# Optimization experiments

Measured on AMD Instinct MI355X. Metric: run time of the kernel, lower is better.

The kernel has to match this reference:

```python
import jax, jax.numpy as jnp
import numpy as np

B, T, C, H = 4, 2048, 1024, 16


def setup_inputs() -> dict:
    key = jax.random.key(0)
    k0, k1, k2 = jax.random.split(key, 3)
    s = C ** -0.5
    return {
        "x": jax.random.normal(k0, (B, T, C), jnp.float32),
        "Wqkv": jax.random.normal(k1, (C, 3 * C), jnp.float32) * s,
        "bqkv": jnp.zeros((3 * C,), jnp.float32),
        "Wo": jax.random.normal(k2, (C, C), jnp.float32) * s,
        "bo": jnp.zeros((C,), jnp.float32),
        "decoder": 1,
    }


def reference(x, Wqkv, bqkv, Wo, bo, decoder):
    Bx, Tx, Cx = x.shape
    d = Cx // H  # head dim
    qkv = x @ Wqkv + bqkv  # [B,T,3C]
    q, k, v = jnp.split(qkv, 3, axis=-1)
    q = q.reshape(Bx, Tx, H, d).transpose(0, 2, 1, 3)  # [B,H,T,d]
    k = k.reshape(Bx, Tx, H, d).transpose(0, 2, 1, 3)
    v = v.reshape(Bx, Tx, H, d).transpose(0, 2, 1, 3)
    # Source: qk / embd_dim**(-0.5)  ==  qk * sqrt(embd_dim)  (faithful quirk)
    scale = jnp.asarray(Cx ** 0.5, x.dtype)
    qk = jnp.einsum("bhqd,bhkd->bhqk", q, k) * scale  # [B,H,T,T]
    if decoder:  # decoder is a Python int constant
        tril = jnp.tril(jnp.ones((Tx, Tx), bool))
        qk = jnp.where(tril, qk, -jnp.inf)
    attn = jax.nn.softmax(qk, axis=-1)
    out = jnp.einsum("bhqk,bhkd->bhqd", attn, v)  # [B,H,T,d]
    out = out.transpose(0, 2, 1, 3).reshape(Bx, Tx, Cx)
    return out @ Wo + bo
```

## Files before the change

### kernel.cpp

```cpp
#include <hip/hip_runtime.h>
#include <cstdint>
#include <cstddef>

#define T_SEQ 2048
#define CEMB  1024
#define NHEAD 16
#define DHEAD 64

#define QSCALE 46.1662413084468f

typedef __attribute__((ext_vector_type(8))) short bf16x8;
typedef __attribute__((ext_vector_type(4))) float f32x4;

static __device__ __forceinline__ unsigned short f2bf(float x) {
    unsigned u = __builtin_bit_cast(unsigned, x);
    unsigned r = (u + 0x7FFFu + ((u >> 16) & 1u)) >> 16;
    return (unsigned short)r;
}
static __device__ __forceinline__ float bf2f(unsigned short b) {
    unsigned u = ((unsigned)b) << 16;
    return __builtin_bit_cast(float, u);
}

static __device__ __forceinline__ void gload16(const short* gsrc, short* ldsbase) {
    __builtin_amdgcn_global_load_lds(
        (const __attribute__((address_space(1))) void*)gsrc,
        (__attribute__((address_space(3))) void*)ldsbase, 16, 0, 0);
}

template<int SPLIT, bool A_F32, int OUT_MODE>
__global__ __launch_bounds__(256) void gemm_mfma_kernel(
    const float* __restrict__ Af, const short* __restrict__ Ah,
    const short* __restrict__ Bh, const short* __restrict__ Bl,
    const float* __restrict__ bias,
    void* __restrict__ Cout, void* __restrict__ Cout2, int K, int ldc)
{
    __shared__ __align__(16) short smem[(SPLIT == 3) ? 16384 : 8192];

    const int tid = threadIdx.x;
    const int w = tid >> 6, l = tid & 63;
    const int lr = l & 15, lg = l >> 4;
    const int wr = w >> 1, wc = w & 1;
    const int row0 = blockIdx.y * 128;
    const int col0 = blockIdx.x * 128;

    f32x4 acc[4][4];
    #pragma unroll
    for (int mt = 0; mt < 4; ++mt)
        #pragma unroll
        for (int nt = 0; nt < 4; ++nt)
            acc[mt][nt] = (f32x4){0.f, 0.f, 0.f, 0.f};

    const int sB0 = w * 128 + l, sB1 = sB0 + 64;
    const short* gB0 = Bh + (size_t)(col0 + (sB0 & 127)) * K + (sB0 >> 7) * 8;
    const short* gB1 = Bh + (size_t)(col0 + (sB1 & 127)) * K + (sB1 >> 7) * 8;
    short* dB0 = &smem[4096 + (w * 128) * 8];
    short* dB1 = &smem[4096 + (w * 128 + 64) * 8];
    const short* gBl0 = nullptr; const short* gBl1 = nullptr;
    if constexpr (SPLIT == 3) {
        gBl0 = Bl + (size_t)(col0 + (sB0 & 127)) * K + (sB0 >> 7) * 8;
        gBl1 = Bl + (size_t)(col0 + (sB1 & 127)) * K + (sB1 >> 7) * 8;
    }
    const short* gA0 = nullptr; const short* gA1 = nullptr;
    if constexpr (!A_F32) {
        gA0 = Ah + (size_t)(row0 + (sB0 & 127)) * K + (sB0 >> 7) * 8;
        gA1 = Ah + (size_t)(row0 + (sB1 & 127)) * K + (sB1 >> 7) * 8;
    }
    short* dA0 = &smem[(w * 128) * 8];
    short* dA1 = &smem[(w * 128 + 64) * 8];

    const int arow = tid >> 1, ahalf = tid & 1;
    const float* gAf = A_F32 ? (Af + (size_t)(row0 + arow) * K + ahalf * 16) : nullptr;

    for (int kt = 0; kt < K; kt += 32) {
        __syncthreads();
        if constexpr (!A_F32) {
            gload16(gA0 + kt, dA0);
            gload16(gA1 + kt, dA1);
        }
        gload16(gB0 + kt, dB0);
        gload16(gB1 + kt, dB1);
        if constexpr (SPLIT == 3) {
            gload16(gBl0 + kt, &smem[12288 + (w * 128) * 8]);
            gload16(gBl1 + kt, &smem[12288 + (w * 128 + 64) * 8]);
        }
        if constexpr (A_F32) {
            const float* src = gAf + kt;
            float4 f0 = *(const float4*)(src);
            float4 f1 = *(const float4*)(src + 4);
            float4 f2 = *(const float4*)(src + 8);
            float4 f3 = *(const float4*)(src + 12);
            float xs[16] = {f0.x, f0.y, f0.z, f0.w, f1.x, f1.y, f1.z, f1.w,
                            f2.x, f2.y, f2.z, f2.w, f3.x, f3.y, f3.z, f3.w};
            #pragma unroll
            for (int q = 0; q < 2; ++q) {
                bf16x8 h8, l8;
                #pragma unroll
                for (int e = 0; e < 8; ++e) {
                    float x = xs[q * 8 + e];
                    if constexpr (SPLIT == 3) {
                        unsigned u = __builtin_bit_cast(unsigned, x);
                        h8[e] = (short)(unsigned short)(u >> 16);
                        float hf = __builtin_bit_cast(float, u & 0xFFFF0000u);
                        l8[e] = (short)f2bf(x - hf);
                    } else {
                        h8[e] = (short)f2bf(x);
                    }
                }
                int slot = (ahalf * 2 + q) * 128 + arow;
                *(bf16x8*)&smem[slot * 8] = h8;
                if constexpr (SPLIT == 3) *(bf16x8*)&smem[8192 + slot * 8] = l8;
            }
        }
        __syncthreads();

        const int aoff = (lg * 128 + wr * 64 + lr) * 8;
        const int boff = 4096 + (lg * 128 + wc * 64 + lr) * 8;
        bf16x8 ahf[4], alf[4];
        #pragma unroll
        for (int mt = 0; mt < 4; ++mt) {
            ahf[mt] = *(const bf16x8*)&smem[aoff + mt * 128];
            if constexpr (SPLIT == 3)
                alf[mt] = *(const bf16x8*)&smem[8192 + aoff + mt * 128];
        }
        #pragma unroll
        for (int nt = 0; nt < 4; ++nt) {
            bf16x8 bhf = *(const bf16x8*)&smem[boff + nt * 128];
            if constexpr (SPLIT == 3) {
                bf16x8 blf = *(const bf16x8*)&smem[8192 + boff + nt * 128];
                #pragma unroll
                for (int mt = 0; mt < 4; ++mt) {
                    acc[mt][nt] = __builtin_amdgcn_mfma_f32_16x16x32_bf16(ahf[mt], bhf, acc[mt][nt], 0, 0, 0);
                    acc[mt][nt] = __builtin_amdgcn_mfma_f32_16x16x32_bf16(alf[mt], bhf, acc[mt][nt], 0, 0, 0);
                    acc[mt][nt] = __builtin_amdgcn_mfma_f32_16x16x32_bf16(ahf[mt], blf, acc[mt][nt], 0, 0, 0);
                }
            } else {
                #pragma unroll
                for (int mt = 0; mt < 4; ++mt)
                    acc[mt][nt] = __builtin_amdgcn_mfma_f32_16x16x32_bf16(ahf[mt], bhf, acc[mt][nt], 0, 0, 0);
            }
        }
    }

    #pragma unroll
    for (int mt = 0; mt < 4; ++mt) {
        #pragma unroll
        for (int r = 0; r < 4; ++r) {
            int m = row0 + wr * 64 + mt * 16 + lg * 4 + r;
            #pragma unroll
            for (int nt = 0; nt < 4; ++nt) {
                int n = col0 + wc * 64 + nt * 16 + lr;
                float v = acc[mt][nt][r] + bias[n];
                if constexpr (OUT_MODE == 0) {
                    ((float*)Cout)[(size_t)m * ldc + n] = v;
                } else if constexpr (OUT_MODE == 1) {
                    ((short*)Cout)[(size_t)m * ldc + n] = (short)f2bf(v);
                } else {
                    if (n < 1024) v *= QSCALE;
                    unsigned u = __builtin_bit_cast(unsigned, v);
                    ((short*)Cout)[(size_t)m * ldc + n] = (short)(unsigned short)(u >> 16);
                    float hf = __builtin_bit_cast(float, u & 0xFFFF0000u);
                    ((short*)Cout2)[(size_t)m * ldc + n] = (short)f2bf(v - hf);
                }
            }
        }
    }
}

__global__ __launch_bounds__(256) void transpose_split_kernel(
    const float* __restrict__ src, int nsrc,
    short* __restrict__ hi, short* __restrict__ lo)
{
    __shared__ float tile[64][68];
    const int tid = threadIdx.x;
    const int n0 = blockIdx.x * 64, k0 = blockIdx.y * 64;
    {
        int kr = tid >> 2, cg = tid & 3;
        const float* s = src + (size_t)(k0 + kr) * nsrc + n0 + cg * 16;
        #pragma unroll
        for (int q = 0; q < 4; ++q) {
            float4 f = *(const float4*)(s + q * 4);
            tile[kr][cg * 16 + q * 4 + 0] = f.x;
            tile[kr][cg * 16 + q * 4 + 1] = f.y;
            tile[kr][cg * 16 + q * 4 + 2] = f.z;
            tile[kr][cg * 16 + q * 4 + 3] = f.w;
        }
    }
    __syncthreads();
    {
        int nr = tid >> 2, kg = tid & 3;
        int n = n0 + nr;
        bf16x8 h0, h1, lo0, lo1;
        #pragma unroll
        for (int e = 0; e < 8; ++e) {
            float a = tile[kg * 16 + e][nr];
            float b = tile[kg * 16 + 8 + e][nr];
            unsigned short ha = f2bf(a), hb = f2bf(b);
            h0[e] = (short)ha; h1[e] = (short)hb;
            lo0[e] = (short)f2bf(a - bf2f(ha));
            lo1[e] = (short)f2bf(b - bf2f(hb));
        }
        short* dh = hi + (size_t)n * 1024 + k0 + kg * 16;
        *(bf16x8*)dh = h0;
        *(bf16x8*)(dh + 8) = h1;
        if (lo) {
            short* dl = lo + (size_t)n * 1024 + k0 + kg * 16;
            *(bf16x8*)dl = lo0;
            *(bf16x8*)(dl + 8) = lo1;
        }
    }
}

__global__ __launch_bounds__(256) void repack_vt_kernel(
    const short* __restrict__ v, short* __restrict__ vt)
{
    __shared__ short tile[64][80];
    const int tid = threadIdx.x;
    const int tt = blockIdx.x, h = blockIdx.y, b = blockIdx.z;
    const int t0 = tt * 64;
    {
        int tr = tid >> 2, cgrp = tid & 3;
        const short* src = v + (size_t)(b * T_SEQ + t0 + tr) * CEMB + h * DHEAD + cgrp * 16;
        *(bf16x8*)&tile[tr][cgrp * 16]     = *(const bf16x8*)src;
        *(bf16x8*)&tile[tr][cgrp * 16 + 8] = *(const bf16x8*)(src + 8);
    }
    __syncthreads();
    {
        int d = tid >> 2, tc = tid & 3;
        short s[16];
        #pragma unroll
        for (int e = 0; e < 16; ++e) s[e] = tile[tc * 16 + e][d];
        short* dst = vt + ((size_t)((b * NHEAD + h) * DHEAD + d)) * T_SEQ + t0 + tc * 16;
        bf16x8 v0, v1;
        #pragma unroll
        for (int e = 0; e < 8; ++e) { v0[e] = s[e]; v1[e] = s[8 + e]; }
        *(bf16x8*)dst       = v0;
        *(bf16x8*)(dst + 8) = v1;
    }
}

__global__ __launch_bounds__(256) void attn_mfma_kernel(
    const short* __restrict__ qkhi, const short* __restrict__ qklo,
    const short* __restrict__ vt, short* __restrict__ ctxb)
{
    __shared__ __align__(16) short smem[16384];

    const int tid = threadIdx.x;
    const int w = tid >> 6, l = tid & 63;
    const int lr = l & 15, lg = l >> 4;

    const int bid = blockIdx.x;
    const int p  = bid >> 6;
    const int bh = bid & 63;
    const int h = bh & 15, b = bh >> 4;
    const size_t bT = (size_t)b * T_SEQ;

    const int g0 = w * 128 + l, g1 = g0 + 64;
    const int rg0 = g0 >> 3, rg1 = g1 >> 3;
    const int sc0 = (g0 & 7) ^ (rg0 & 7), sc1 = (g1 & 7) ^ (rg1 & 7);
    short* const dst0 = &smem[(w * 128) * 8];
    short* const dst1 = &smem[(w * 128 + 64) * 8];

    const size_t koff0 = (bT + rg0) * 2048 + 1024 + h * DHEAD + sc0 * 8;
    const size_t koff1 = (bT + rg1) * 2048 + 1024 + h * DHEAD + sc1 * 8;
    const short* const pKh0 = qkhi + koff0;
    const short* const pKh1 = qkhi + koff1;
    const short* const pKl0 = qklo + koff0;
    const short* const pKl1 = qklo + koff1;
    const short* const pV0 = vt + ((size_t)((b * NHEAD + h) * DHEAD) + rg0) * T_SEQ + sc0 * 8;
    const short* const pV1 = vt + ((size_t)((b * NHEAD + h) * DHEAD) + rg1) * T_SEQ + sc1 * 8;

    for (int half = 0; half < 2; ++half) {
        const int xi = half ? (31 - p) : p;
        const int q0 = xi * 64;
        const int qw = q0 + w * 16;

        bf16x8 ahi[2], alo[2];
        #pragma unroll
        for (int kk = 0; kk < 2; ++kk) {
            size_t off = (bT + qw + lr) * 2048 + h * DHEAD + kk * 32 + lg * 8;
            ahi[kk] = *(const bf16x8*)(qkhi + off);
            alo[kk] = *(const bf16x8*)(qklo + off);
        }

        f32x4 O[4];
        #pragma unroll
        for (int dt = 0; dt < 4; ++dt)
            O[dt] = (f32x4){0.f, 0.f, 0.f, 0.f};
        float mrun[4], lrun[4];
        #pragma unroll
        for (int r = 0; r < 4; ++r) { mrun[r] = -3.0e38f; lrun[r] = 0.f; }

        const int nsteps = xi + 1;
        for (int t = 0; t < nsteps; ++t) {
            const int j0 = t * 64;
            __syncthreads();
            gload16(pKh0 + (size_t)j0 * 2048, dst0);
            gload16(pKh1 + (size_t)j0 * 2048, dst1);
            gload16(pKl0 + (size_t)j0 * 2048, dst0 + 4096);
            gload16(pKl1 + (size_t)j0 * 2048, dst1 + 4096);
            gload16(pV0 + j0, dst0 + 8192);
            gload16(pV1 + j0, dst1 + 8192);
            __syncthreads();

            f32x4 S[4];
            #pragma unroll
            for (int ct = 0; ct < 4; ++ct) {
                f32x4 s = (f32x4){0.f, 0.f, 0.f, 0.f};
                #pragma unroll
                for (int kk = 0; kk < 2; ++kk) {
                    int j  = ct * 16 + lr;
                    int ck = kk * 4 + lg;
                    int idx = j * 64 + ((ck ^ (j & 7)) << 3);
                    bf16x8 bh8 = *(bf16x8*)&smem[idx];
                    bf16x8 bl8 = *(bf16x8*)&smem[4096 + idx];
                    s = __builtin_amdgcn_mfma_f32_16x16x32_bf16(ahi[kk], bh8, s, 0, 0, 0);
                    s = __builtin_amdgcn_mfma_f32_16x16x32_bf16(alo[kk], bh8, s, 0, 0, 0);
                    s = __builtin_amdgcn_mfma_f32_16x16x32_bf16(ahi[kk], bl8, s, 0, 0, 0);
                }
                if (j0 + ct * 16 + 15 > qw) {
                    int jabs = j0 + ct * 16 + lr;
                    #pragma unroll
                    for (int r = 0; r < 4; ++r) {
                        int qabs = qw + lg * 4 + r;
                        s[r] = (jabs <= qabs) ? s[r] : -3.0e38f;
                    }
                }
                S[ct] = s;
            }

            float tm[4];
            #pragma unroll
            for (int r = 0; r < 4; ++r) {
                float v = fmaxf(fmaxf(S[0][r], S[1][r]), fmaxf(S[2][r], S[3][r]));
                v = fmaxf(v, __shfl_xor(v, 1));
                v = fmaxf(v, __shfl_xor(v, 2));
                v = fmaxf(v, __shfl_xor(v, 4));
                v = fmaxf(v, __shfl_xor(v, 8));
                tm[r] = v;
            }
            bool exceed = (tm[0] > mrun[0]) | (tm[1] > mrun[1]) |
                          (tm[2] > mrun[2]) | (tm[3] > mrun[3]);
            if (__any(exceed)) {
                #pragma unroll
                for (int r = 0; r < 4; ++r) {
                    float mnew  = fmaxf(mrun[r], tm[r]);
                    float alpha = __builtin_amdgcn_exp2f(mrun[r] - mnew);
                    mrun[r] = mnew;
                    lrun[r] *= alpha;
                    #pragma unroll
                    for (int dt = 0; dt < 4; ++dt)
                        O[dt][r] *= alpha;
                }
            }

            float lsum[4] = {0.f, 0.f, 0.f, 0.f};
            #pragma unroll
            for (int ct = 0; ct < 4; ++ct) {
                #pragma unroll
                for (int r = 0; r < 4; ++r) {
                    float pv = __builtin_amdgcn_exp2f(S[ct][r] - mrun[r]);
                    lsum[r] += pv;
                    int row = lg * 4 + r;
                    int col = ct * 16 + lr;
                    smem[12288 + w * 1024 + row * 64 + (col ^ ((row & 7) << 3))] = (short)f2bf(pv);
                }
            }
            #pragma unroll
            for (int r = 0; r < 4; ++r) {
                float s = lsum[r];
                s += __shfl_xor(s, 1);
                s += __shfl_xor(s, 2);
                s += __shfl_xor(s, 4);
                s += __shfl_xor(s, 8);
                lrun[r] += s;
            }

            __builtin_amdgcn_wave_barrier();

            bf16x8 pa[2];
            #pragma unroll
            for (int jk = 0; jk < 2; ++jk) {
                int ck = jk * 4 + lg;
                pa[jk] = *(bf16x8*)&smem[12288 + w * 1024 + lr * 64 + ((ck ^ (lr & 7)) << 3)];
            }
            #pragma unroll
            for (int dt = 0; dt < 4; ++dt) {
                #pragma unroll
                for (int jk = 0; jk < 2; ++jk) {
                    int d  = dt * 16 + lr;
                    int ck = jk * 4 + lg;
                    bf16x8 vb = *(bf16x8*)&smem[8192 + d * 64 + ((ck ^ (d & 7)) << 3)];
                    O[dt] = __builtin_amdgcn_mfma_f32_16x16x32_bf16(pa[jk], vb, O[dt], 0, 0, 0);
                }
            }
        }

        #pragma unroll
        for (int r = 0; r < 4; ++r) {
            float inv = 1.0f / lrun[r];
            int row = qw + lg * 4 + r;
            #pragma unroll
            for (int dt = 0; dt < 4; ++dt) {
                int col = h * DHEAD + dt * 16 + lr;
                ctxb[(size_t)(b * T_SEQ + row) * CEMB + col] = (short)f2bf(O[dt][r] * inv);
            }
        }
    }
}

extern "C" void kernel_launch(void* const* d_in, const int* in_sizes, int n_in,
                              void* d_out, int out_size, void* d_ws, size_t ws_size,
                              hipStream_t stream)
{
    const float* x    = (const float*)d_in[0];
    const float* Wqkv = (const float*)d_in[1];
    const float* bqkv = (const float*)d_in[2];
    const float* Wo   = (const float*)d_in[3];
    const float* bo   = (const float*)d_in[4];
    float* out = (float*)d_out;

    char* ws = (char*)d_ws;
    short* qkhi = (short*)ws;
    short* vbuf = (short*)ws;
    short* qklo = (short*)(ws + (size_t)(32u << 20));
    short* Vt   = (short*)(ws + (size_t)(64u << 20));
    short* ctxb = (short*)(ws + (size_t)(80u << 20));
    short* WhiT = (short*)(ws + (size_t)(96u << 20));
    short* WloT = (short*)(ws + (size_t)(102u << 20));
    short* WoT  = (short*)(ws + (size_t)(108u << 20));

    transpose_split_kernel<<<dim3(48, 16), 256, 0, stream>>>(Wqkv, 3 * CEMB, WhiT, WloT);
    transpose_split_kernel<<<dim3(16, 16), 256, 0, stream>>>(Wo, CEMB, WoT, nullptr);

    gemm_mfma_kernel<1, true, 1><<<dim3(8, 64), 256, 0, stream>>>(
        x, nullptr, WhiT + (size_t)2048 * 1024, nullptr, bqkv + 2048, vbuf, nullptr, CEMB, CEMB);

    repack_vt_kernel<<<dim3(32, 16, 4), 256, 0, stream>>>(vbuf, Vt);

    gemm_mfma_kernel<3, true, 2><<<dim3(16, 64), 256, 0, stream>>>(
        x, nullptr, WhiT, WloT, bqkv, qkhi, qklo, CEMB, 2048);

    attn_mfma_kernel<<<dim3(1024), 256, 0, stream>>>(qkhi, qklo, Vt, ctxb);

    gemm_mfma_kernel<1, false, 0><<<dim3(8, 64), 256, 0, stream>>>(
        nullptr, ctxb, WoT, nullptr, bo, out, nullptr, CEMB, CEMB);
}
```

Measured before the change: 384.5 us.

## Register-prefetch next K/V tile during attention compute, defer row-sum reduction

Replaces the direct global-to-LDS loads with a register-staged prefetch: the next K-hi/K-lo/V tile is loaded into registers while the current tile's MFMA and softmax work runs, then written to LDS after a barrier. The per-step cross-lane reduction of the softmax denominator is moved to once at the end, and P is stored to LDS by truncation instead of round-to-nearest bf16. The launch bounds now request 4 blocks per CU. The aim is to hide global load latency and cut per-step shuffles, at the cost of more registers, which may limit occupancy, and slightly less accurate P values.

```diff
diff --git a/kernel.cpp b/kernel.cpp
--- a/kernel.cpp
+++ b/kernel.cpp
@@ -239,7 +239,7 @@
     }
 }
 
-__global__ __launch_bounds__(256) void attn_mfma_kernel(
+__global__ __launch_bounds__(256, 4) void attn_mfma_kernel(
     const short* __restrict__ qkhi, const short* __restrict__ qklo,
     const short* __restrict__ vt, short* __restrict__ ctxb)
 {
@@ -255,26 +255,46 @@
     const int h = bh & 15, b = bh >> 4;
     const size_t bT = (size_t)b * T_SEQ;
 
-    const int g0 = w * 128 + l, g1 = g0 + 64;
-    const int rg0 = g0 >> 3, rg1 = g1 >> 3;
-    const int sc0 = (g0 & 7) ^ (rg0 & 7), sc1 = (g1 & 7) ^ (rg1 & 7);
-    short* const dst0 = &smem[(w * 128) * 8];
-    short* const dst1 = &smem[(w * 128 + 64) * 8];
-
-    const size_t koff0 = (bT + rg0) * 2048 + 1024 + h * DHEAD + sc0 * 8;
-    const size_t koff1 = (bT + rg1) * 2048 + 1024 + h * DHEAD + sc1 * 8;
-    const short* const pKh0 = qkhi + koff0;
-    const short* const pKh1 = qkhi + koff1;
-    const short* const pKl0 = qklo + koff0;
-    const short* const pKl1 = qklo + koff1;
-    const short* const pV0 = vt + ((size_t)((b * NHEAD + h) * DHEAD) + rg0) * T_SEQ + sc0 * 8;
-    const short* const pV1 = vt + ((size_t)((b * NHEAD + h) * DHEAD) + rg1) * T_SEQ + sc1 * 8;
+    const int rA = tid >> 3, rB = rA + 32;
+    const int sc = (tid & 7) ^ (rA & 7);
+    const size_t kA = (bT + rA) * 2048 + 1024 + h * DHEAD + sc * 8;
+    const size_t kB = (bT + rB) * 2048 + 1024 + h * DHEAD + sc * 8;
+    const short* const bKhA = qkhi + kA;
+    const short* const bKhB = qkhi + kB;
+    const short* const bKlA = qklo + kA;
+    const short* const bKlB = qklo + kB;
+    const size_t vtb = (size_t)((b * NHEAD + h) * DHEAD);
+    const short* const bVA = vt + (vtb + rA) * T_SEQ + sc * 8;
+    const short* const bVB = vt + (vtb + rB) * T_SEQ + sc * 8;
+
+    bf16x8 stg[6];
+    #define LOADR(jt) do {                                                \
+        size_t ko = (size_t)(jt) * 131072; int vo = (jt) * 64;            \
+        stg[0] = *(const bf16x8*)(bKhA + ko);                             \
+        stg[1] = *(const bf16x8*)(bKhB + ko);                             \
+        stg[2] = *(const bf16x8*)(bKlA + ko);                             \
+        stg[3] = *(const bf16x8*)(bKlB + ko);                             \
+        stg[4] = *(const bf16x8*)(bVA + vo);                              \
+        stg[5] = *(const bf16x8*)(bVB + vo);                              \
+    } while (0)
+    #define WRITER() do {                                                 \
+        *(bf16x8*)&smem[tid * 8]         = stg[0];                        \
+        *(bf16x8*)&smem[tid * 8 + 2048]  = stg[1];                        \
+        *(bf16x8*)&smem[tid * 8 + 4096]  = stg[2];                        \
+        *(bf16x8*)&smem[tid * 8 + 6144]  = stg[3];                        \
+        *(bf16x8*)&smem[tid * 8 + 8192]  = stg[4];                        \
+        *(bf16x8*)&smem[tid * 8 + 10240] = stg[5];                        \
+    } while (0)
 
     for (int half = 0; half < 2; ++half) {
         const int xi = half ? (31 - p) : p;
         const int q0 = xi * 64;
         const int qw = q0 + w * 16;
 
+        LOADR(0);
+        __syncthreads();
+        WRITER();
+
         bf16x8 ahi[2], alo[2];
         #pragma unroll
         for (int kk = 0; kk < 2; ++kk) {
@@ -287,21 +307,17 @@
         #pragma unroll
         for (int dt = 0; dt < 4; ++dt)
             O[dt] = (f32x4){0.f, 0.f, 0.f, 0.f};
-        float mrun[4], lrun[4];
-        #pragma unroll
-        for (int r = 0; r < 4; ++r) { mrun[r] = -3.0e38f; lrun[r] = 0.f; }
+        float mrun[4], lpart[4];
+        #pragma unroll
+        for (int r = 0; r < 4; ++r) { mrun[r] = -3.0e38f; lpart[r] = 0.f; }
+
+        __syncthreads();
 
         const int nsteps = xi + 1;
         for (int t = 0; t < nsteps; ++t) {
             const int j0 = t * 64;
-            __syncthreads();
-            gload16(pKh0 + (size_t)j0 * 2048, dst0);
-            gload16(pKh1 + (size_t)j0 * 2048, dst1);
-            gload16(pKl0 + (size_t)j0 * 2048, dst0 + 4096);
-            gload16(pKl1 + (size_t)j0 * 2048, dst1 + 4096);
-            gload16(pV0 + j0, dst0 + 8192);
-            gload16(pV1 + j0, dst1 + 8192);
-            __syncthreads();
+            const bool pf = (t + 1 < nsteps);
+            if (pf) LOADR(t + 1);
 
             f32x4 S[4];
             #pragma unroll
@@ -347,33 +363,24 @@
                     float mnew  = fmaxf(mrun[r], tm[r]);
                     float alpha = __builtin_amdgcn_exp2f(mrun[r] - mnew);
                     mrun[r] = mnew;
-                    lrun[r] *= alpha;
+                    lpart[r] *= alpha;
                     #pragma unroll
                     for (int dt = 0; dt < 4; ++dt)
                         O[dt][r] *= alpha;
                 }
             }
 
-            float lsum[4] = {0.f, 0.f, 0.f, 0.f};
             #pragma unroll
             for (int ct = 0; ct < 4; ++ct) {
                 #pragma unroll
                 for (int r = 0; r < 4; ++r) {
                     float pv = __builtin_amdgcn_exp2f(S[ct][r] - mrun[r]);
-                    lsum[r] += pv;
+                    lpart[r] += pv;
                     int row = lg * 4 + r;
                     int col = ct * 16 + lr;
-                    smem[12288 + w * 1024 + row * 64 + (col ^ ((row & 7) << 3))] = (short)f2bf(pv);
-                }
-            }
-            #pragma unroll
-            for (int r = 0; r < 4; ++r) {
-                float s = lsum[r];
-                s += __shfl_xor(s, 1);
-                s += __shfl_xor(s, 2);
-                s += __shfl_xor(s, 4);
-                s += __shfl_xor(s, 8);
-                lrun[r] += s;
+                    smem[12288 + w * 1024 + row * 64 + (col ^ ((row & 7) << 3))] =
+                        (short)(unsigned short)(__builtin_bit_cast(unsigned, pv) >> 16);
+                }
             }
 
             __builtin_amdgcn_wave_barrier();
@@ -394,11 +401,22 @@
                     O[dt] = __builtin_amdgcn_mfma_f32_16x16x32_bf16(pa[jk], vb, O[dt], 0, 0, 0);
                 }
             }
+
+            __syncthreads();
+            if (pf) {
+                WRITER();
+                __syncthreads();
+            }
         }
 
         #pragma unroll
         for (int r = 0; r < 4; ++r) {
-            float inv = 1.0f / lrun[r];
+            float s = lpart[r];
+            s += __shfl_xor(s, 1);
+            s += __shfl_xor(s, 2);
+            s += __shfl_xor(s, 4);
+            s += __shfl_xor(s, 8);
+            float inv = 1.0f / s;
             int row = qw + lg * 4 + r;
             #pragma unroll
             for (int dt = 0; dt < 4; ++dt) {
@@ -407,6 +425,8 @@
             }
         }
     }
+    #undef LOADR
+    #undef WRITER
 }
 
 extern "C" void kernel_launch(void* const* d_in, const int* in_sizes, int n_in,
```

New measurement: 374.5 us. 2.6% less time.
